# Performance work log

Hardware: AMD Instinct MI355X
Metric: run time of the kernel (lower is better)

The kernel has to match this reference:

```python
import jax, jax.numpy as jnp
import numpy as np

BSZ, D = 256, 512
LOGIT_SCALE = 1.0


def setup_inputs() -> dict:
    key = jax.random.key(0)
    k1, k2, k3 = jax.random.split(key, 3)
    x = jax.random.normal(k1, (BSZ, D), dtype=jnp.float32)
    y = jax.random.normal(k2, (BSZ, D), dtype=jnp.float32)
    z = jax.random.normal(k3, (BSZ, D), dtype=jnp.float32)
    return {"x": x, "y": y, "z": z}


def _logits_n_squared(anchor, a, b, shift):
    # torch recursion: products[i*bsz + r] = a[r] * roll(b, i)[r] = a[r] * b[(r - i) % bsz]
    bsz = anchor.shape[0]
    P = a[None, :, :] * b[shift]              # (i, r, d) = (bsz, bsz, d)
    logits = jnp.einsum('ad,ird->air', anchor, P)  # (a, i, r)
    return LOGIT_SCALE * logits.reshape(bsz, bsz * bsz)


def _cross_entropy_diag(logits):
    bsz = logits.shape[0]
    lp = jax.nn.log_softmax(logits, axis=-1)
    idx = jnp.arange(bsz)
    return -jnp.mean(lp[idx, idx])


def reference(x, y, z):
    bsz = x.shape[0]
    r = jnp.arange(bsz)
    shift = (r[None, :] - r[:, None]) % bsz   # (i, r): index into b after roll by i
    reps = [x, y, z]
    losses = []
    for i in range(3):
        anchor = reps[i]
        non_anchor = [reps[j] for j in range(3) if j != i]
        logits = _logits_n_squared(anchor, non_anchor[0], non_anchor[1], shift)
        losses.append(_cross_entropy_diag(logits))
    return sum(losses) / 3.0
```

## Files before the change

### kernel.cpp

```cpp
#include <hip/hip_runtime.h>

#define DIM 512
#define BK 32

typedef unsigned int uint;
typedef unsigned short ushort;
typedef __attribute__((ext_vector_type(8))) short short8;
typedef __attribute__((ext_vector_type(4))) float f32x4;

__device__ __forceinline__ uint pack_bf16(float a, float b) {
    union { float f; uint u; } ua, ub;
    ua.f = a; ub.f = b;
    uint x0 = ua.u + 0x8000u;
    uint x1 = ub.u + 0x8000u;
    return __builtin_amdgcn_perm(x1, x0, 0x07060302);
}

__global__ void zconv_kernel(const float* __restrict__ z, ushort* __restrict__ zb) {
    int t = blockIdx.x * 256 + threadIdx.x;
    int f = t * 8;
    float4 a = *(const float4*)(z + f);
    float4 b = *(const float4*)(z + f + 4);
    uint4 o;
    o.x = pack_bf16(a.x, a.y);
    o.y = pack_bf16(a.z, a.w);
    o.z = pack_bf16(b.x, b.y);
    o.w = pack_bf16(b.z, b.w);
    *(uint4*)(zb + f) = o;
}

__global__ void diag_kernel(const float* __restrict__ x, const float* __restrict__ y,
                            const float* __restrict__ z, float* __restrict__ diag) {
    int a = blockIdx.x;
    int l = threadIdx.x;
    float s = 0.f;
    for (int d = l; d < DIM; d += 64)
        s += x[a * DIM + d] * y[a * DIM + d] * z[a * DIM + d];
    #pragma unroll
    for (int m = 1; m < 64; m <<= 1) s += __shfl_xor(s, m, 64);
    if (l == 0) diag[a] = s;
}

__global__ void gemm_kernel(const float* __restrict__ x, const float* __restrict__ y,
                            const ushort* __restrict__ zb,
                            float* __restrict__ rowM, float* __restrict__ rowS,
                            float* __restrict__ colM, float* __restrict__ colS) {
    __shared__ __align__(16) float xs[DIM];
    __shared__ __align__(16) ushort As[128 * BK];
    __shared__ __align__(16) ushort Bs[256 * BK];
    __shared__ float redA[128 * 4];
    __shared__ float rowMaxS[128];
    __shared__ float redB[256 * 2];
    __shared__ float colMaxS[256];

    const int tid = threadIdx.x;
    const int a   = blockIdx.x >> 1;
    const int rt  = blockIdx.x & 1;

    xs[tid] = x[a * DIM + tid];

    const int lane = tid & 63;
    const int wave = tid >> 6;
    const int quad = lane >> 4;
    const int ln15 = lane & 15;
    const int wr = wave >> 2;
    const int wc = wave & 3;

    f32x4 acc[4][4];
    #pragma unroll
    for (int i = 0; i < 4; ++i)
        #pragma unroll
        for (int j = 0; j < 4; ++j)
            acc[i][j] = (f32x4){0.f, 0.f, 0.f, 0.f};

    const int fA = tid * 8;
    const int rA = fA >> 5;
    const int kA = fA & 31;
    const float* yrow = y + (rt * 128 + rA) * DIM + kA;

    for (int kt = 0; kt < DIM / BK; ++kt) {
        const int k0 = kt * BK;
        __syncthreads();
        {
            float4 y0 = *(const float4*)(yrow + k0);
            float4 y1 = *(const float4*)(yrow + k0 + 4);
            float4 x0 = *(const float4*)(xs + k0 + kA);
            float4 x1 = *(const float4*)(xs + k0 + kA + 4);
            uint4 o;
            o.x = pack_bf16(y0.x * x0.x, y0.y * x0.y);
            o.y = pack_bf16(y0.z * x0.z, y0.w * x0.w);
            o.z = pack_bf16(y1.x * x1.x, y1.y * x1.y);
            o.w = pack_bf16(y1.z * x1.z, y1.w * x1.w);
            *(uint4*)(As + fA) = o;
        }
        #pragma unroll
        for (int h = 0; h < 2; ++h) {
            int f = h * 4096 + tid * 8;
            int s = f >> 5;
            int kk = f & 31;
            uint4 v = *(const uint4*)(zb + s * DIM + k0 + kk);
            *(uint4*)(Bs + f) = v;
        }
        __syncthreads();
        short8 af[4], bfr[4];
        #pragma unroll
        for (int i = 0; i < 4; ++i)
            af[i] = *(const short8*)(As + (wr * 64 + i * 16 + ln15) * BK + quad * 8);
        #pragma unroll
        for (int j = 0; j < 4; ++j)
            bfr[j] = *(const short8*)(Bs + (wc * 64 + j * 16 + ln15) * BK + quad * 8);
        #pragma unroll
        for (int i = 0; i < 4; ++i)
            #pragma unroll
            for (int j = 0; j < 4; ++j)
                acc[i][j] = __builtin_amdgcn_mfma_f32_16x16x32_bf16(af[i], bfr[j], acc[i][j], 0, 0, 0);
    }
    __syncthreads();

    #pragma unroll
    for (int i = 0; i < 4; ++i) {
        #pragma unroll
        for (int reg = 0; reg < 4; ++reg) {
            float m = fmaxf(fmaxf(acc[i][0][reg], acc[i][1][reg]),
                            fmaxf(acc[i][2][reg], acc[i][3][reg]));
            #pragma unroll
            for (int d = 1; d < 16; d <<= 1) m = fmaxf(m, __shfl_xor(m, d, 64));
            if (ln15 == 0) redA[(wr * 64 + i * 16 + quad * 4 + reg) * 4 + wc] = m;
        }
    }
    __syncthreads();
    if (tid < 128) {
        float m = fmaxf(fmaxf(redA[tid * 4 + 0], redA[tid * 4 + 1]),
                        fmaxf(redA[tid * 4 + 2], redA[tid * 4 + 3]));
        rowMaxS[tid] = m;
    }
    __syncthreads();
    #pragma unroll
    for (int i = 0; i < 4; ++i) {
        #pragma unroll
        for (int reg = 0; reg < 4; ++reg) {
            int r = wr * 64 + i * 16 + quad * 4 + reg;
            float rm = rowMaxS[r];
            float s = __expf(acc[i][0][reg] - rm) + __expf(acc[i][1][reg] - rm)
                    + __expf(acc[i][2][reg] - rm) + __expf(acc[i][3][reg] - rm);
            #pragma unroll
            for (int d = 1; d < 16; d <<= 1) s += __shfl_xor(s, d, 64);
            if (ln15 == 0) redA[r * 4 + wc] = s;
        }
    }
    __syncthreads();
    if (tid < 128) {
        float s = redA[tid * 4 + 0] + redA[tid * 4 + 1] + redA[tid * 4 + 2] + redA[tid * 4 + 3];
        int rg = rt * 128 + tid;
        rowM[a * 256 + rg] = rowMaxS[tid];
        rowS[a * 256 + rg] = s;
    }

    #pragma unroll
    for (int j = 0; j < 4; ++j) {
        float m = -3.4e38f;
        #pragma unroll
        for (int i = 0; i < 4; ++i)
            #pragma unroll
            for (int reg = 0; reg < 4; ++reg)
                m = fmaxf(m, acc[i][j][reg]);
        m = fmaxf(m, __shfl_xor(m, 16, 64));
        m = fmaxf(m, __shfl_xor(m, 32, 64));
        if (quad == 0) redB[(wc * 64 + j * 16 + ln15) * 2 + wr] = m;
    }
    __syncthreads();
    if (tid < 256) colMaxS[tid] = fmaxf(redB[tid * 2], redB[tid * 2 + 1]);
    __syncthreads();
    #pragma unroll
    for (int j = 0; j < 4; ++j) {
        int n = wc * 64 + j * 16 + ln15;
        float cm = colMaxS[n];
        float s = 0.f;
        #pragma unroll
        for (int i = 0; i < 4; ++i)
            #pragma unroll
            for (int reg = 0; reg < 4; ++reg)
                s += __expf(acc[i][j][reg] - cm);
        s += __shfl_xor(s, 16, 64);
        s += __shfl_xor(s, 32, 64);
        if (quad == 0) redB[n * 2 + wr] = s;
    }
    __syncthreads();
    if (tid < 256) {
        float s = redB[tid * 2] + redB[tid * 2 + 1];
        colM[(a * 256 + tid) * 2 + rt] = colMaxS[tid];
        colS[(a * 256 + tid) * 2 + rt] = s;
    }
}

__device__ __forceinline__ float blk_max(float v, float* sm) {
    #pragma unroll
    for (int d = 1; d < 64; d <<= 1) v = fmaxf(v, __shfl_xor(v, d, 64));
    __syncthreads();
    if ((threadIdx.x & 63) == 0) sm[threadIdx.x >> 6] = v;
    __syncthreads();
    return fmaxf(fmaxf(sm[0], sm[1]), fmaxf(sm[2], sm[3]));
}
__device__ __forceinline__ float blk_sum(float v, float* sm) {
    #pragma unroll
    for (int d = 1; d < 64; d <<= 1) v += __shfl_xor(v, d, 64);
    __syncthreads();
    if ((threadIdx.x & 63) == 0) sm[threadIdx.x >> 6] = v;
    __syncthreads();
    return sm[0] + sm[1] + sm[2] + sm[3];
}

__global__ void combine_kernel(const float* __restrict__ rowM, const float* __restrict__ rowS,
                               const float* __restrict__ colM, const float* __restrict__ colS,
                               float* __restrict__ m123) {
    __shared__ float sm[4];
    int b = blockIdx.x, t = threadIdx.x;
    float m = rowM[b * 256 + t], s = rowS[b * 256 + t];
    float M = blk_max(m, sm);
    float S = blk_sum(s * __expf(m - M), sm);
    float M1 = M + __logf(S);
    m = rowM[t * 256 + b]; s = rowS[t * 256 + b];
    M = blk_max(m, sm);
    S = blk_sum(s * __expf(m - M), sm);
    float M2 = M + __logf(S);
    float am = colM[(t * 256 + b) * 2 + 0], av = colS[(t * 256 + b) * 2 + 0];
    float bm = colM[(t * 256 + b) * 2 + 1], bv = colS[(t * 256 + b) * 2 + 1];
    m = fmaxf(am, bm);
    s = av * __expf(am - m) + bv * __expf(bm - m);
    M = blk_max(m, sm);
    S = blk_sum(s * __expf(m - M), sm);
    float M3 = M + __logf(S);
    if (t == 0) m123[b] = M1 + M2 + M3;
}

__global__ void final_kernel(const float* __restrict__ m123, const float* __restrict__ diag,
                             float* __restrict__ out) {
    __shared__ float sm[4];
    int t = threadIdx.x;
    float S1 = blk_sum(m123[t], sm);
    float S2 = blk_sum(diag[t], sm);
    if (t == 0) out[0] = S1 / 768.0f - S2 / 256.0f;
}

extern "C" void kernel_launch(void* const* d_in, const int* in_sizes, int n_in,
                              void* d_out, int out_size, void* d_ws, size_t ws_size,
                              hipStream_t stream) {
    const float* x = (const float*)d_in[0];
    const float* y = (const float*)d_in[1];
    const float* z = (const float*)d_in[2];
    char* w = (char*)d_ws;
    ushort* zb  = (ushort*)(w);
    float*  rowM = (float*)(w + 262144);
    float*  rowS = (float*)(w + 524288);
    float*  colM = (float*)(w + 786432);
    float*  colS = (float*)(w + 1310720);
    float*  diag = (float*)(w + 1835008);
    float*  m123 = (float*)(w + 1836032);
    float*  out  = (float*)d_out;

    zconv_kernel<<<64, 256, 0, stream>>>(z, zb);
    diag_kernel<<<256, 64, 0, stream>>>(x, y, z, diag);
    gemm_kernel<<<512, 512, 0, stream>>>(x, y, zb, rowM, rowS, colM, colS);
    combine_kernel<<<256, 256, 0, stream>>>(rowM, rowS, colM, colS, m123);
    final_kernel<<<1, 256, 0, stream>>>(m123, diag, out);
}
```

Before: 99.77 us.

## Fuse z conversion and diagonal into GEMM, merge final reduction into combine

Removes the separate z-to-bf16 and diagonal kernels: the GEMM now converts fp32 z on the fly when staging B tiles and computes the diagonal in the rt==0 blocks. The final scalar reduction is folded into the combine kernel using an atomic counter so that the last block finishes the sum. This cuts the launch count from five to two and drops the bf16 z round-trip through memory. In exchange every GEMM block re-reads and re-converts all of z in fp32, which doubles B-side global traffic, and a launch_bounds hint is added.

```diff
diff --git a/kernel.cpp b/kernel.cpp
--- a/kernel.cpp
+++ b/kernel.cpp
@@ -16,35 +16,12 @@
     return __builtin_amdgcn_perm(x1, x0, 0x07060302);
 }
 
-__global__ void zconv_kernel(const float* __restrict__ z, ushort* __restrict__ zb) {
-    int t = blockIdx.x * 256 + threadIdx.x;
-    int f = t * 8;
-    float4 a = *(const float4*)(z + f);
-    float4 b = *(const float4*)(z + f + 4);
-    uint4 o;
-    o.x = pack_bf16(a.x, a.y);
-    o.y = pack_bf16(a.z, a.w);
-    o.z = pack_bf16(b.x, b.y);
-    o.w = pack_bf16(b.z, b.w);
-    *(uint4*)(zb + f) = o;
-}
-
-__global__ void diag_kernel(const float* __restrict__ x, const float* __restrict__ y,
-                            const float* __restrict__ z, float* __restrict__ diag) {
-    int a = blockIdx.x;
-    int l = threadIdx.x;
-    float s = 0.f;
-    for (int d = l; d < DIM; d += 64)
-        s += x[a * DIM + d] * y[a * DIM + d] * z[a * DIM + d];
-    #pragma unroll
-    for (int m = 1; m < 64; m <<= 1) s += __shfl_xor(s, m, 64);
-    if (l == 0) diag[a] = s;
-}
-
-__global__ void gemm_kernel(const float* __restrict__ x, const float* __restrict__ y,
-                            const ushort* __restrict__ zb,
-                            float* __restrict__ rowM, float* __restrict__ rowS,
-                            float* __restrict__ colM, float* __restrict__ colS) {
+__global__ void __launch_bounds__(512, 4)
+gemm_fused(const float* __restrict__ x, const float* __restrict__ y,
+           const float* __restrict__ z,
+           float* __restrict__ rowM, float* __restrict__ rowS,
+           float* __restrict__ colM, float* __restrict__ colS,
+           float* __restrict__ diag, uint* __restrict__ counter) {
     __shared__ __align__(16) float xs[DIM];
     __shared__ __align__(16) ushort As[128 * BK];
     __shared__ __align__(16) ushort Bs[256 * BK];
@@ -52,10 +29,13 @@
     __shared__ float rowMaxS[128];
     __shared__ float redB[256 * 2];
     __shared__ float colMaxS[256];
+    __shared__ float dred[8];
 
     const int tid = threadIdx.x;
     const int a   = blockIdx.x >> 1;
     const int rt  = blockIdx.x & 1;
+
+    if (blockIdx.x == 0 && tid == 0) *counter = 0u;
 
     xs[tid] = x[a * DIM + tid];
 
@@ -66,6 +46,20 @@
     const int wr = wave >> 2;
     const int wc = wave & 3;
 
+    if (rt == 0) {
+        float p = xs[tid] * y[a * DIM + tid] * z[a * DIM + tid];
+        #pragma unroll
+        for (int m = 1; m < 64; m <<= 1) p += __shfl_xor(p, m, 64);
+        if (lane == 0) dred[wave] = p;
+        __syncthreads();
+        if (tid == 0) {
+            float s = 0.f;
+            #pragma unroll
+            for (int w2 = 0; w2 < 8; ++w2) s += dred[w2];
+            diag[a] = s;
+        }
+    }
+
     f32x4 acc[4][4];
     #pragma unroll
     for (int i = 0; i < 4; ++i)
@@ -77,6 +71,11 @@
     const int rA = fA >> 5;
     const int kA = fA & 31;
     const float* yrow = y + (rt * 128 + rA) * DIM + kA;
+
+    const int fB = tid * 16;
+    const int sB = fB >> 5;
+    const int kB = fB & 31;
+    const float* zrow = z + sB * DIM + kB;
 
     for (int kt = 0; kt < DIM / BK; ++kt) {
         const int k0 = kt * BK;
@@ -93,13 +92,22 @@
             o.w = pack_bf16(y1.z * x1.z, y1.w * x1.w);
             *(uint4*)(As + fA) = o;
         }
-        #pragma unroll
-        for (int h = 0; h < 2; ++h) {
-            int f = h * 4096 + tid * 8;
-            int s = f >> 5;
-            int kk = f & 31;
-            uint4 v = *(const uint4*)(zb + s * DIM + k0 + kk);
-            *(uint4*)(Bs + f) = v;
+        {
+            float4 z0 = *(const float4*)(zrow + k0);
+            float4 z1 = *(const float4*)(zrow + k0 + 4);
+            float4 z2 = *(const float4*)(zrow + k0 + 8);
+            float4 z3 = *(const float4*)(zrow + k0 + 12);
+            uint4 o0, o1;
+            o0.x = pack_bf16(z0.x, z0.y);
+            o0.y = pack_bf16(z0.z, z0.w);
+            o0.z = pack_bf16(z1.x, z1.y);
+            o0.w = pack_bf16(z1.z, z1.w);
+            o1.x = pack_bf16(z2.x, z2.y);
+            o1.y = pack_bf16(z2.z, z2.w);
+            o1.z = pack_bf16(z3.x, z3.y);
+            o1.w = pack_bf16(z3.z, z3.w);
+            *(uint4*)(Bs + fB) = o0;
+            *(uint4*)(Bs + fB + 8) = o1;
         }
         __syncthreads();
         short8 af[4], bfr[4];
@@ -210,10 +218,13 @@
     return sm[0] + sm[1] + sm[2] + sm[3];
 }
 
-__global__ void combine_kernel(const float* __restrict__ rowM, const float* __restrict__ rowS,
-                               const float* __restrict__ colM, const float* __restrict__ colS,
-                               float* __restrict__ m123) {
+__global__ void combine_final(const float* __restrict__ rowM, const float* __restrict__ rowS,
+                              const float* __restrict__ colM, const float* __restrict__ colS,
+                              const float* __restrict__ diag,
+                              float* __restrict__ m123, uint* __restrict__ counter,
+                              float* __restrict__ out) {
     __shared__ float sm[4];
+    __shared__ uint isLast;
     int b = blockIdx.x, t = threadIdx.x;
     float m = rowM[b * 256 + t], s = rowS[b * 256 + t];
     float M = blk_max(m, sm);
@@ -230,16 +241,20 @@
     M = blk_max(m, sm);
     S = blk_sum(s * __expf(m - M), sm);
     float M3 = M + __logf(S);
-    if (t == 0) m123[b] = M1 + M2 + M3;
-}
-
-__global__ void final_kernel(const float* __restrict__ m123, const float* __restrict__ diag,
-                             float* __restrict__ out) {
-    __shared__ float sm[4];
-    int t = threadIdx.x;
-    float S1 = blk_sum(m123[t], sm);
-    float S2 = blk_sum(diag[t], sm);
-    if (t == 0) out[0] = S1 / 768.0f - S2 / 256.0f;
+    if (t == 0) {
+        m123[b] = M1 + M2 + M3;
+        __threadfence();
+        isLast = (atomicAdd(counter, 1u) == 255u) ? 1u : 0u;
+    }
+    __syncthreads();
+    if (isLast) {
+        __threadfence();
+        const volatile float* vm = (const volatile float*)m123;
+        const volatile float* vd = (const volatile float*)diag;
+        float S1 = blk_sum(vm[t], sm);
+        float S2 = blk_sum(vd[t], sm);
+        if (t == 0) out[0] = S1 / 768.0f - S2 / 256.0f;
+    }
 }
 
 extern "C" void kernel_launch(void* const* d_in, const int* in_sizes, int n_in,
@@ -249,18 +264,15 @@
     const float* y = (const float*)d_in[1];
     const float* z = (const float*)d_in[2];
     char* w = (char*)d_ws;
-    ushort* zb  = (ushort*)(w);
-    float*  rowM = (float*)(w + 262144);
-    float*  rowS = (float*)(w + 524288);
-    float*  colM = (float*)(w + 786432);
-    float*  colS = (float*)(w + 1310720);
-    float*  diag = (float*)(w + 1835008);
-    float*  m123 = (float*)(w + 1836032);
-    float*  out  = (float*)d_out;
-
-    zconv_kernel<<<64, 256, 0, stream>>>(z, zb);
-    diag_kernel<<<256, 64, 0, stream>>>(x, y, z, diag);
-    gemm_kernel<<<512, 512, 0, stream>>>(x, y, zb, rowM, rowS, colM, colS);
-    combine_kernel<<<256, 256, 0, stream>>>(rowM, rowS, colM, colS, m123);
-    final_kernel<<<1, 256, 0, stream>>>(m123, diag, out);
-}
+    float* rowM = (float*)(w);
+    float* rowS = (float*)(w + 262144);
+    float* colM = (float*)(w + 524288);
+    float* colS = (float*)(w + 1048576);
+    float* diag = (float*)(w + 1572864);
+    float* m123 = (float*)(w + 1573888);
+    uint*  counter = (uint*)(w + 1574912);
+    float* out  = (float*)d_out;
+
+    gemm_fused<<<512, 512, 0, stream>>>(x, y, z, rowM, rowS, colM, colS, diag, counter);
+    combine_final<<<256, 256, 0, stream>>>(rowM, rowS, colM, colS, diag, m123, counter, out);
+}
```

Measured after the change: 103.9 us. +4.1%, slower.
